# Kernel tuning notes

Measured on AMD Instinct MI355X. Metric: run time of the kernel, lower is better.

The kernel has to match this reference:

```python
import jax, jax.numpy as jnp
import numpy as np

N = 100_000      # nodes
E = 1_600_000    # edges (before self loops)
IN = 128         # in_dim
HID = 64         # hidden_dim (per head)
HEADS = 2
NEG_SLOPE = 0.2  # PyG GATConv default negative_slope


def setup_inputs() -> dict:
    key = jax.random.key(0)
    k = jax.random.split(key, 6)
    x = jax.random.normal(k[0], (N, IN), jnp.float32)
    edge_index = jax.random.randint(k[1], (2, E), 0, N, dtype=jnp.int64)
    # GATConv linear (no bias in lin, bias added after aggregation in PyG)
    W = jax.random.normal(k[2], (IN, HEADS * HID), jnp.float32) * (1.0 / np.sqrt(IN))
    att_src = jax.random.normal(k[3], (HEADS, HID), jnp.float32) * 0.1
    att_dst = jax.random.normal(k[4], (HEADS, HID), jnp.float32) * 0.1
    bias = jnp.zeros((HEADS * HID,), jnp.float32)
    prelu_w = jnp.full((HEADS * HID,), 0.25, jnp.float32)  # nn.PReLU default init
    return {"x": x, "edge_index": edge_index, "W": W, "att_src": att_src,
            "att_dst": att_dst, "bias": bias, "prelu_w": prelu_w}


def reference(x, edge_index, W, att_src, att_dst, bias, prelu_w):
    n = x.shape[0]
    h = (x @ W).reshape(n, HEADS, HID)                 # [N,H,C]
    a_s = jnp.einsum('nhc,hc->nh', h, att_src)         # [N,H]
    a_d = jnp.einsum('nhc,hc->nh', h, att_dst)         # [N,H]
    # add self loops (PyG default add_self_loops=True)
    loops = jnp.arange(n, dtype=edge_index.dtype)
    src = jnp.concatenate([edge_index[0], loops])      # [Et]
    dst = jnp.concatenate([edge_index[1], loops])      # [Et]
    logits = a_s[src] + a_d[dst]                       # [Et,H]
    logits = jnp.where(logits >= 0, logits, NEG_SLOPE * logits)  # LeakyReLU
    # segment softmax over destination neighborhoods
    m = jax.ops.segment_max(logits, dst, num_segments=n)         # [N,H]
    e = jnp.exp(logits - m[dst])
    s = jax.ops.segment_sum(e, dst, num_segments=n)              # [N,H]
    alpha = e / (s[dst] + 1e-16)                                 # [Et,H]
    # (attention dropout p=0.2 is identity in eval mode)
    msg = h[src] * alpha[..., None]                    # [Et,H,C]
    out = jax.ops.segment_sum(msg, dst, num_segments=n).reshape(n, HEADS * HID)
    out = out + bias
    # PReLU with per-channel weight
    return jnp.where(out >= 0, out, prelu_w * out)
```

## Files before the change

kernel.cpp:

```cpp
#include <hip/hip_runtime.h>
#include <hip/hip_fp16.h>
#include <hip/hip_bf16.h>
#include <cstdint>
#include <cstddef>

#define NEG_SLOPE 0.2f
#define BSH 8
#define BNODES 256
#define CAP 5120

typedef __attribute__((ext_vector_type(8))) short short8v;
typedef __attribute__((ext_vector_type(4))) float f32x4;
typedef __attribute__((ext_vector_type(2))) uint32_t u32x2;

__device__ __forceinline__ uint32_t bf16pair(float a, float b) {
    __hip_bfloat162 h = __float22bfloat162_rn(make_float2(a, b));
    return *reinterpret_cast<uint32_t*>(&h);
}
__device__ __forceinline__ uint16_t rne16(float f) {
    uint32_t u = __float_as_uint(f);
    return (uint16_t)((u + 0x7fffu + ((u >> 16) & 1u)) >> 16);
}
__device__ __forceinline__ float bflo(uint32_t u) { return __uint_as_float(u << 16); }
__device__ __forceinline__ float bfhi(uint32_t u) { return __uint_as_float(u & 0xffff0000u); }
__device__ __forceinline__ uint32_t packf16(float a, float b) {
    __half2 h = __floats2half2_rn(a, b);
    return *reinterpret_cast<uint32_t*>(&h);
}

__global__ __launch_bounds__(256, 3) void gemm_scatter(
    const float* __restrict__ x, const float* __restrict__ W,
    const float* __restrict__ att_src, const float* __restrict__ att_dst,
    uint32_t* __restrict__ hb, float* __restrict__ a_s, float* __restrict__ a_d,
    const int* __restrict__ src, const int* __restrict__ dst,
    int* __restrict__ gcur, uint32_t* __restrict__ pairs,
    int e, int nb, int n, int nbs)
{
    constexpr int PW = 136;
    __shared__ __align__(16) char smem[52224];
    const int tid = threadIdx.x;

    if (blockIdx.x < nbs) {
        int* histL  = (int*)smem;
        int* gbaseL = histL + 512;
        const int t0 = blockIdx.x * 4096;

        for (int i = tid; i < nb; i += 256) histL[i] = 0;
        __syncthreads();

        int      myb[16];
        int      myslot[16];
        uint32_t mypk[16];
#pragma unroll 16
        for (int k = 0; k < 16; ++k) {
            int i = t0 + tid + k * 256;
            if (i < e) {
                int s = __builtin_nontemporal_load(src + i);
                int d = __builtin_nontemporal_load(dst + i);
                int b = d >> BSH;
                myb[k]    = b;
                mypk[k]   = (uint32_t)s | ((uint32_t)(d & (BNODES - 1)) << 17);
                myslot[k] = atomicAdd(&histL[b], 1);
            } else myb[k] = -1;
        }
        __syncthreads();
        for (int i = tid; i < nb; i += 256) {
            int c = histL[i];
            gbaseL[i] = c ? atomicAdd(&gcur[i], c) : 0;
        }
        __syncthreads();
#pragma unroll 16
        for (int k = 0; k < 16; ++k) {
            if (myb[k] >= 0) {
                int p = gbaseL[myb[k]] + myslot[k];
                if (p < CAP) pairs[(size_t)myb[k] * CAP + p] = mypk[k];
            }
        }
        return;
    }

    unsigned short* Wt = (unsigned short*)smem;
    unsigned short* Hs = (unsigned short*)(smem + 34816);
    const int w    = tid >> 6;
    const int lane = tid & 63;
    const int cl   = lane & 15;
    const int gq   = lane >> 4;
    const int base = (blockIdx.x - nbs) * 64;

    const float4* W4 = (const float4*)W;
#pragma unroll
    for (int i = 0; i < 8; ++i) {
        int idx = tid + i * 256;
        int k   = (idx >> 5) * 2, c4 = (idx & 31) * 4;
        float4 v0 = W4[k * 32 + (idx & 31)];
        float4 v1 = W4[(k + 1) * 32 + (idx & 31)];
        *(uint32_t*)&Wt[(c4 + 0) * PW + k] = bf16pair(v0.x, v1.x);
        *(uint32_t*)&Wt[(c4 + 1) * PW + k] = bf16pair(v0.y, v1.y);
        *(uint32_t*)&Wt[(c4 + 2) * PW + k] = bf16pair(v0.z, v1.z);
        *(uint32_t*)&Wt[(c4 + 3) * PW + k] = bf16pair(v0.w, v1.w);
    }

    float asr[8], adr[8];
#pragma unroll
    for (int t = 0; t < 8; ++t) {
        asr[t] = att_src[t * 16 + cl];
        adr[t] = att_dst[t * 16 + cl];
    }
    __syncthreads();

    const int rowg = base + w * 16 + cl;
    const int rowc = rowg < n ? rowg : (n - 1);
    const f32x4* xp = (const f32x4*)(x + (size_t)rowc * 128);

    f32x4 acc[8];
#pragma unroll
    for (int t = 0; t < 8; ++t) acc[t] = (f32x4){0.f, 0.f, 0.f, 0.f};

#pragma unroll
    for (int s = 0; s < 4; ++s) {
        int kq = s * 8 + gq * 2;
        f32x4 f0 = __builtin_nontemporal_load(xp + kq);
        f32x4 f1 = __builtin_nontemporal_load(xp + kq + 1);
        union { short8v v; uint32_t d[4]; } A;
        A.d[0] = bf16pair(f0.x, f0.y);
        A.d[1] = bf16pair(f0.z, f0.w);
        A.d[2] = bf16pair(f1.x, f1.y);
        A.d[3] = bf16pair(f1.z, f1.w);
#pragma unroll
        for (int t = 0; t < 8; ++t) {
            union { short8v v; uint4 q; } B;
            B.q = *(const uint4*)&Wt[(t * 16 + cl) * PW + s * 32 + gq * 8];
            acc[t] = __builtin_amdgcn_mfma_f32_16x16x32_bf16(A.v, B.v, acc[t], 0, 0, 0);
        }
    }

    float ps0[4], ps1[4], pd0[4], pd1[4];
#pragma unroll
    for (int r = 0; r < 4; ++r) { ps0[r] = ps1[r] = pd0[r] = pd1[r] = 0.f; }
#pragma unroll
    for (int t = 0; t < 8; ++t) {
#pragma unroll
        for (int r = 0; r < 4; ++r) {
            float v = acc[t][r];
            if (t < 4) { ps0[r] = fmaf(v, asr[t], ps0[r]); pd0[r] = fmaf(v, adr[t], pd0[r]); }
            else       { ps1[r] = fmaf(v, asr[t], ps1[r]); pd1[r] = fmaf(v, adr[t], pd1[r]); }
        }
    }
#pragma unroll
    for (int off = 1; off < 16; off <<= 1) {
#pragma unroll
        for (int r = 0; r < 4; ++r) {
            ps0[r] += __shfl_xor(ps0[r], off);
            ps1[r] += __shfl_xor(ps1[r], off);
            pd0[r] += __shfl_xor(pd0[r], off);
            pd1[r] += __shfl_xor(pd1[r], off);
        }
    }
    if (cl == 0) {
#pragma unroll
        for (int r = 0; r < 4; ++r) {
            int rg = base + w * 16 + gq * 4 + r;
            if (rg < n) {
                a_s[rg * 2 + 0] = ps0[r]; a_s[rg * 2 + 1] = ps1[r];
                a_d[rg * 2 + 0] = pd0[r]; a_d[rg * 2 + 1] = pd1[r];
            }
        }
    }

#pragma unroll
    for (int t = 0; t < 8; ++t) {
#pragma unroll
        for (int r = 0; r < 4; ++r) {
            int row = gq * 4 + r;
            Hs[(size_t)w * 16 * PW + row * PW + t * 16 + cl] = rne16(acc[t][r]);
        }
    }
    __syncthreads();
#pragma unroll
    for (int q = 0; q < 4; ++q) {
        int row = q * 4 + gq;
        int cu  = 4 * cl;
        uint4 v = *(const uint4*)&Hs[(size_t)w * 16 * PW + row * PW + cu * 2];
        int rg = base + w * 16 + row;
        if (rg < n) *(uint4*)&hb[(size_t)rg * 64 + cu] = v;
    }
}

__global__ __launch_bounds__(512) void build_csr(
    const uint32_t* __restrict__ pairs, const int* __restrict__ gcur,
    const float* __restrict__ a_s, const float* __restrict__ a_d,
    uint32_t* __restrict__ meta, uint2* __restrict__ edges, int n, int nb)
{
    __shared__ uint32_t pl[CAP];
    __shared__ int degL[BNODES], curL[BNODES];
    __shared__ float adL[BNODES * 2];
    __shared__ int bscan[512];
    __shared__ int wsum8[8];
    const int b = blockIdx.x, tid = threadIdx.x;
    const int lane = tid & 63, wid = tid >> 6;
    const int nbase = b * BNODES;
    const int nodes = min(BNODES, n - nbase);

    int tot = 0;
    if (tid < nb) {
        int nn = min(BNODES, n - tid * BNODES);
        tot = min(gcur[tid], CAP) + nn;
    }
    int sc = tot;
#pragma unroll
    for (int off = 1; off < 64; off <<= 1) {
        int t = __shfl_up(sc, off);
        if (lane >= off) sc += t;
    }
    if (lane == 63) wsum8[wid] = sc;
    __syncthreads();
    {
        int woff = 0;
#pragma unroll
        for (int k = 0; k < 8; ++k) woff += (k < wid) ? wsum8[k] : 0;
        bscan[tid] = sc + woff;
    }
    if (tid < BNODES) degL[tid] = 1;
    float es0 = 0.f, es1 = 0.f;
    if (tid < nodes) {
        int g = nbase + tid;
        float2 ad = ((const float2*)a_d)[g];
        adL[2 * tid]     = ad.x;
        adL[2 * tid + 1] = ad.y;
        float2 as = ((const float2*)a_s)[g];
        float l0 = as.x + ad.x; l0 = l0 >= 0.f ? l0 : NEG_SLOPE * l0;
        float l1 = as.y + ad.y; l1 = l1 >= 0.f ? l1 : NEG_SLOPE * l1;
        es0 = __expf(l0); es1 = __expf(l1);
    }
    __syncthreads();
    const int C    = min(gcur[b], CAP);
    const int base = bscan[b] - (C + nodes);

    for (int i = tid; i < C; i += 512) {
        uint32_t p = __builtin_nontemporal_load(pairs + (size_t)b * CAP + i);
        pl[i] = p;
        atomicAdd(&degL[p >> 17], 1);
    }
    __syncthreads();

    int v = (tid < nodes) ? degL[tid] : 0;
    int sc2 = v;
#pragma unroll
    for (int off = 1; off < 64; off <<= 1) {
        int t = __shfl_up(sc2, off);
        if (lane >= off) sc2 += t;
    }
    if (lane == 63 && tid < BNODES) wsum8[wid] = sc2;
    __syncthreads();
    int woff2 = 0;
#pragma unroll
    for (int k = 0; k < 4; ++k) woff2 += (k < wid) ? wsum8[k] : 0;
    const int exc = sc2 - v + woff2;

    if (tid < nodes) {
        edges[base + exc] = make_uint2((uint32_t)(nbase + tid), packf16(es0, es1));
        curL[tid] = exc + 1;
        meta[nbase + tid] = (uint32_t)(base + exc) | ((uint32_t)v << 24);
    }
    __syncthreads();
    for (int i = tid; i < C; i += 512) {
        uint32_t p  = pl[i];
        int dl  = p >> 17;
        int s   = p & 0x1FFFF;
        float2 as = ((const float2*)a_s)[s];
        float l0 = as.x + adL[2 * dl];     l0 = l0 >= 0.f ? l0 : NEG_SLOPE * l0;
        float l1 = as.y + adL[2 * dl + 1]; l1 = l1 >= 0.f ? l1 : NEG_SLOPE * l1;
        float e0 = __expf(l0), e1 = __expf(l1);
        int pos = atomicAdd(&curL[dl], 1);
        edges[base + pos] = make_uint2((uint32_t)s, packf16(e0, e1));
    }
}

__global__ __launch_bounds__(256) void attn_agg(
    const uint32_t* __restrict__ hb, const uint2* __restrict__ edges,
    const uint32_t* __restrict__ meta,
    const float* __restrict__ bias, const float* __restrict__ prelu_w,
    float* __restrict__ out, int n)
{
    const int gw   = (blockIdx.x * blockDim.x + threadIdx.x) >> 6;
    const int lane = threadIdx.x & 63;
    if (gw >= n) return;
    const uint32_t mt = meta[gw];
    const int start = (int)(mt & 0xFFFFFFu);
    const int deg   = (int)(mt >> 24);

    if (deg <= 64) {
        int sv = 0; float e0 = 0.f, e1 = 0.f;
        if (lane < deg) {
            u32x2 ed = __builtin_nontemporal_load((const u32x2*)(edges + start + lane));
            sv = (int)ed.x;
            uint32_t ey = ed.y;
            __half2 h2 = *reinterpret_cast<__half2*>(&ey);
            e0 = __half2float(__low2half(h2));
            e1 = __half2float(__high2half(h2));
        }
        float s0 = e0, s1 = e1;
#pragma unroll
        for (int off = 32; off > 0; off >>= 1) {
            s0 += __shfl_xor(s0, off);
            s1 += __shfl_xor(s1, off);
        }
        const float inv0 = 1.f / (s0 + 1e-16f);
        const float inv1 = 1.f / (s1 + 1e-16f);

        const int g = lane >> 4, r = lane & 15;
        float acc[8];
#pragma unroll
        for (int q = 0; q < 8; ++q) acc[q] = 0.f;

        const uint4* hb4 = (const uint4*)hb;
        const int iters = (deg + 15) >> 4;
        for (int jj = 0; jj < iters; ++jj) {
            const int j0 = jj * 16 + g;
            int   s0v = __shfl(sv, j0);
            int   s1v = __shfl(sv, j0 + 4);
            int   s2v = __shfl(sv, j0 + 8);
            int   s3v = __shfl(sv, j0 + 12);
            float A00 = __shfl(e0, j0),      A10 = __shfl(e1, j0);
            float A01 = __shfl(e0, j0 + 4),  A11 = __shfl(e1, j0 + 4);
            float A02 = __shfl(e0, j0 + 8),  A12 = __shfl(e1, j0 + 8);
            float A03 = __shfl(e0, j0 + 12), A13 = __shfl(e1, j0 + 12);
            float Aa = (r < 8) ? A00 : A10;
            float Ab = (r < 8) ? A01 : A11;
            float Ac = (r < 8) ? A02 : A12;
            float Ad = (r < 8) ? A03 : A13;
            uint4 qa = hb4[(size_t)s0v * 16 + r];
            uint4 qb = hb4[(size_t)s1v * 16 + r];
            uint4 qc = hb4[(size_t)s2v * 16 + r];
            uint4 qd = hb4[(size_t)s3v * 16 + r];
            acc[0] = fmaf(Aa, bflo(qa.x), acc[0]); acc[1] = fmaf(Aa, bfhi(qa.x), acc[1]);
            acc[2] = fmaf(Aa, bflo(qa.y), acc[2]); acc[3] = fmaf(Aa, bfhi(qa.y), acc[3]);
            acc[4] = fmaf(Aa, bflo(qa.z), acc[4]); acc[5] = fmaf(Aa, bfhi(qa.z), acc[5]);
            acc[6] = fmaf(Aa, bflo(qa.w), acc[6]); acc[7] = fmaf(Aa, bfhi(qa.w), acc[7]);
            acc[0] = fmaf(Ab, bflo(qb.x), acc[0]); acc[1] = fmaf(Ab, bfhi(qb.x), acc[1]);
            acc[2] = fmaf(Ab, bflo(qb.y), acc[2]); acc[3] = fmaf(Ab, bfhi(qb.y), acc[3]);
            acc[4] = fmaf(Ab, bflo(qb.z), acc[4]); acc[5] = fmaf(Ab, bfhi(qb.z), acc[5]);
            acc[6] = fmaf(Ab, bflo(qb.w), acc[6]); acc[7] = fmaf(Ab, bfhi(qb.w), acc[7]);
            acc[0] = fmaf(Ac, bflo(qc.x), acc[0]); acc[1] = fmaf(Ac, bfhi(qc.x), acc[1]);
            acc[2] = fmaf(Ac, bflo(qc.y), acc[2]); acc[3] = fmaf(Ac, bfhi(qc.y), acc[3]);
            acc[4] = fmaf(Ac, bflo(qc.z), acc[4]); acc[5] = fmaf(Ac, bfhi(qc.z), acc[5]);
            acc[6] = fmaf(Ac, bflo(qc.w), acc[6]); acc[7] = fmaf(Ac, bfhi(qc.w), acc[7]);
            acc[0] = fmaf(Ad, bflo(qd.x), acc[0]); acc[1] = fmaf(Ad, bfhi(qd.x), acc[1]);
            acc[2] = fmaf(Ad, bflo(qd.y), acc[2]); acc[3] = fmaf(Ad, bfhi(qd.y), acc[3]);
            acc[4] = fmaf(Ad, bflo(qd.z), acc[4]); acc[5] = fmaf(Ad, bfhi(qd.z), acc[5]);
            acc[6] = fmaf(Ad, bflo(qd.w), acc[6]); acc[7] = fmaf(Ad, bfhi(qd.w), acc[7]);
        }
#pragma unroll
        for (int q = 0; q < 8; ++q) {
            acc[q] += __shfl_xor(acc[q], 16);
            acc[q] += __shfl_xor(acc[q], 32);
        }
        if (lane < 16) {
            const float winv = (lane < 8) ? inv0 : inv1;
            float4 b0 = ((const float4*)bias)[lane * 2];
            float4 b1 = ((const float4*)bias)[lane * 2 + 1];
            float4 p0 = ((const float4*)prelu_w)[lane * 2];
            float4 p1 = ((const float4*)prelu_w)[lane * 2 + 1];
            f32x4 w0, w1;
            w0.x = fmaf(acc[0], winv, b0.x); w0.x = w0.x >= 0.f ? w0.x : p0.x * w0.x;
            w0.y = fmaf(acc[1], winv, b0.y); w0.y = w0.y >= 0.f ? w0.y : p0.y * w0.y;
            w0.z = fmaf(acc[2], winv, b0.z); w0.z = w0.z >= 0.f ? w0.z : p0.z * w0.z;
            w0.w = fmaf(acc[3], winv, b0.w); w0.w = w0.w >= 0.f ? w0.w : p0.w * w0.w;
            w1.x = fmaf(acc[4], winv, b1.x); w1.x = w1.x >= 0.f ? w1.x : p1.x * w1.x;
            w1.y = fmaf(acc[5], winv, b1.y); w1.y = w1.y >= 0.f ? w1.y : p1.y * w1.y;
            w1.z = fmaf(acc[6], winv, b1.z); w1.z = w1.z >= 0.f ? w1.z : p1.z * w1.z;
            w1.w = fmaf(acc[7], winv, b1.w); w1.w = w1.w >= 0.f ? w1.w : p1.w * w1.w;
            float* op = out + (size_t)gw * 128 + lane * 8;
            __builtin_nontemporal_store(w0, (f32x4*)op);
            __builtin_nontemporal_store(w1, (f32x4*)(op + 4));
        }
    } else {
        float s0 = 0.f, s1 = 0.f;
        for (int t = lane; t < deg; t += 64) {
            uint32_t ey = edges[start + t].y;
            __half2 h2 = *reinterpret_cast<__half2*>(&ey);
            s0 += __half2float(__low2half(h2));
            s1 += __half2float(__high2half(h2));
        }
#pragma unroll
        for (int off = 32; off > 0; off >>= 1) {
            s0 += __shfl_xor(s0, off);
            s1 += __shfl_xor(s1, off);
        }
        const float inv0 = 1.f / (s0 + 1e-16f);
        const float inv1 = 1.f / (s1 + 1e-16f);

        float accL = 0.f, accH = 0.f;
        for (int t0 = 0; t0 < deg; t0 += 64) {
            int tt = t0 + lane;
            int sv = 0; float e0 = 0.f, e1 = 0.f;
            if (tt < deg) {
                uint2 ed = edges[start + tt];
                sv = (int)ed.x;
                __half2 h2 = *reinterpret_cast<__half2*>(&ed.y);
                e0 = __half2float(__low2half(h2));
                e1 = __half2float(__high2half(h2));
            }
            int kmax = min(64, deg - t0);
            for (int j = 0; j < kmax; ++j) {
                int   s  = __shfl(sv, j);
                float A0 = __shfl(e0, j);
                float A1 = __shfl(e1, j);
                float A  = (lane < 32) ? A0 : A1;
                uint32_t u = hb[(size_t)s * 64 + lane];
                accL = fmaf(A, bflo(u), accL);
                accH = fmaf(A, bfhi(u), accH);
            }
        }
        const float winv = (lane < 32) ? inv0 : inv1;
        float2 bz = ((const float2*)bias)[lane];
        float2 pw = ((const float2*)prelu_w)[lane];
        float o0 = fmaf(accL, winv, bz.x), o1 = fmaf(accH, winv, bz.y);
        o0 = o0 >= 0.f ? o0 : pw.x * o0;
        o1 = o1 >= 0.f ? o1 : pw.y * o1;
        float2 rr; rr.x = o0; rr.y = o1;
        ((float2*)out)[(size_t)gw * 64 + lane] = rr;
    }
}

extern "C" void kernel_launch(void* const* d_in, const int* in_sizes, int n_in,
                              void* d_out, int out_size, void* d_ws, size_t ws_size,
                              hipStream_t stream)
{
    const float* x        = (const float*)d_in[0];
    const int*   ei       = (const int*)d_in[1];
    const float* W        = (const float*)d_in[2];
    const float* att_src  = (const float*)d_in[3];
    const float* att_dst  = (const float*)d_in[4];
    const float* bias     = (const float*)d_in[5];
    const float* prelu_w  = (const float*)d_in[6];
    float* out = (float*)d_out;

    const int n = in_sizes[0] / 128;
    const int e = in_sizes[1] / 2;
    const int* srcp = ei;
    const int* dstp = ei + e;
    const int nb  = (n + BNODES - 1) / BNODES;
    const int nbs = (e + 4095) / 4096;
    const int nbg = (n + 63) / 64;

    uint32_t* hb    = (uint32_t*)d_ws;
    uint32_t* meta  = (uint32_t*)(hb + (size_t)n * 64);
    float*    a_s   = (float*)(meta + n);
    float*    a_d   = a_s + (size_t)n * 2;
    int*      gcur  = (int*)(a_d + (size_t)n * 2);
    uint32_t* pairs = (uint32_t*)(gcur + 512);
    uint2*    edges = (uint2*)(pairs + (size_t)nb * CAP);

    hipMemsetAsync(gcur, 0, 512 * sizeof(int), stream);
    gemm_scatter<<<nbs + nbg, 256, 0, stream>>>(x, W, att_src, att_dst,
                                                hb, a_s, a_d, srcp, dstp,
                                                gcur, pairs, e, nb, n, nbs);
    build_csr<<<nb, 512, 0, stream>>>(pairs, gcur, a_s, a_d, meta, edges, n, nb);
    attn_agg<<<(n + 3) / 4, 256, 0, stream>>>(hb, edges, meta, bias, prelu_w, out, n);
}
```

Baseline: 141.4 us.

## Process two destination nodes per wavefront in attention aggregation

```diff
diff --git a/kernel.cpp b/kernel.cpp
--- a/kernel.cpp
+++ b/kernel.cpp
@@ -282,17 +282,22 @@
     const float* __restrict__ bias, const float* __restrict__ prelu_w,
     float* __restrict__ out, int n)
 {
-    const int gw   = (blockIdx.x * blockDim.x + threadIdx.x) >> 6;
+    const int wv   = (blockIdx.x * blockDim.x + threadIdx.x) >> 6;
     const int lane = threadIdx.x & 63;
-    if (gw >= n) return;
-    const uint32_t mt = meta[gw];
+    const int gwA  = wv * 2;
+    if (gwA >= n) return;
+    const int h = lane >> 5, hlane = lane & 31;
+    const int gw = gwA + h;
+    const bool act = gw < n;
+    const uint32_t mt = act ? meta[gw] : 0u;
     const int start = (int)(mt & 0xFFFFFFu);
-    const int deg   = (int)(mt >> 24);
-
-    if (deg <= 64) {
+    const int deg   = act ? (int)(mt >> 24) : 0;
+    const uint4* hb4 = (const uint4*)hb;
+
+    if (__all(deg <= 32)) {
         int sv = 0; float e0 = 0.f, e1 = 0.f;
-        if (lane < deg) {
-            u32x2 ed = __builtin_nontemporal_load((const u32x2*)(edges + start + lane));
+        if (hlane < deg) {
+            u32x2 ed = __builtin_nontemporal_load((const u32x2*)(edges + start + hlane));
             sv = (int)ed.x;
             uint32_t ey = ed.y;
             __half2 h2 = *reinterpret_cast<__half2*>(&ey);
@@ -301,30 +306,30 @@
         }
         float s0 = e0, s1 = e1;
 #pragma unroll
-        for (int off = 32; off > 0; off >>= 1) {
+        for (int off = 16; off > 0; off >>= 1) {
             s0 += __shfl_xor(s0, off);
             s1 += __shfl_xor(s1, off);
         }
         const float inv0 = 1.f / (s0 + 1e-16f);
         const float inv1 = 1.f / (s1 + 1e-16f);
 
-        const int g = lane >> 4, r = lane & 15;
+        const int g = (lane >> 4) & 1, r = lane & 15;
+        const int sbase = h * 32;
         float acc[8];
 #pragma unroll
         for (int q = 0; q < 8; ++q) acc[q] = 0.f;
 
-        const uint4* hb4 = (const uint4*)hb;
-        const int iters = (deg + 15) >> 4;
+        const int iters = (deg + 7) >> 3;
         for (int jj = 0; jj < iters; ++jj) {
-            const int j0 = jj * 16 + g;
-            int   s0v = __shfl(sv, j0);
-            int   s1v = __shfl(sv, j0 + 4);
-            int   s2v = __shfl(sv, j0 + 8);
-            int   s3v = __shfl(sv, j0 + 12);
-            float A00 = __shfl(e0, j0),      A10 = __shfl(e1, j0);
-            float A01 = __shfl(e0, j0 + 4),  A11 = __shfl(e1, j0 + 4);
-            float A02 = __shfl(e0, j0 + 8),  A12 = __shfl(e1, j0 + 8);
-            float A03 = __shfl(e0, j0 + 12), A13 = __shfl(e1, j0 + 12);
+            const int j0 = jj * 8 + g * 4;
+            int   s0v = __shfl(sv, sbase + j0);
+            int   s1v = __shfl(sv, sbase + j0 + 1);
+            int   s2v = __shfl(sv, sbase + j0 + 2);
+            int   s3v = __shfl(sv, sbase + j0 + 3);
+            float A00 = __shfl(e0, sbase + j0),     A10 = __shfl(e1, sbase + j0);
+            float A01 = __shfl(e0, sbase + j0 + 1), A11 = __shfl(e1, sbase + j0 + 1);
+            float A02 = __shfl(e0, sbase + j0 + 2), A12 = __shfl(e1, sbase + j0 + 2);
+            float A03 = __shfl(e0, sbase + j0 + 3), A13 = __shfl(e1, sbase + j0 + 3);
             float Aa = (r < 8) ? A00 : A10;
             float Ab = (r < 8) ? A01 : A11;
             float Ac = (r < 8) ? A02 : A12;
@@ -351,16 +356,14 @@
             acc[6] = fmaf(Ad, bflo(qd.w), acc[6]); acc[7] = fmaf(Ad, bfhi(qd.w), acc[7]);
         }
 #pragma unroll
-        for (int q = 0; q < 8; ++q) {
-            acc[q] += __shfl_xor(acc[q], 16);
-            acc[q] += __shfl_xor(acc[q], 32);
-        }
-        if (lane < 16) {
-            const float winv = (lane < 8) ? inv0 : inv1;
-            float4 b0 = ((const float4*)bias)[lane * 2];
-            float4 b1 = ((const float4*)bias)[lane * 2 + 1];
-            float4 p0 = ((const float4*)prelu_w)[lane * 2];
-            float4 p1 = ((const float4*)prelu_w)[lane * 2 + 1];
+        for (int q = 0; q < 8; ++q) acc[q] += __shfl_xor(acc[q], 16);
+
+        if (hlane < 16 && act) {
+            const float winv = (r < 8) ? inv0 : inv1;
+            float4 b0 = ((const float4*)bias)[r * 2];
+            float4 b1 = ((const float4*)bias)[r * 2 + 1];
+            float4 p0 = ((const float4*)prelu_w)[r * 2];
+            float4 p1 = ((const float4*)prelu_w)[r * 2 + 1];
             f32x4 w0, w1;
             w0.x = fmaf(acc[0], winv, b0.x); w0.x = w0.x >= 0.f ? w0.x : p0.x * w0.x;
             w0.y = fmaf(acc[1], winv, b0.y); w0.y = w0.y >= 0.f ? w0.y : p0.y * w0.y;
@@ -370,56 +373,147 @@
             w1.y = fmaf(acc[5], winv, b1.y); w1.y = w1.y >= 0.f ? w1.y : p1.y * w1.y;
             w1.z = fmaf(acc[6], winv, b1.z); w1.z = w1.z >= 0.f ? w1.z : p1.z * w1.z;
             w1.w = fmaf(acc[7], winv, b1.w); w1.w = w1.w >= 0.f ? w1.w : p1.w * w1.w;
-            float* op = out + (size_t)gw * 128 + lane * 8;
+            float* op = out + (size_t)gw * 128 + r * 8;
             __builtin_nontemporal_store(w0, (f32x4*)op);
             __builtin_nontemporal_store(w1, (f32x4*)(op + 4));
         }
-    } else {
-        float s0 = 0.f, s1 = 0.f;
-        for (int t = lane; t < deg; t += 64) {
-            uint32_t ey = edges[start + t].y;
-            __half2 h2 = *reinterpret_cast<__half2*>(&ey);
-            s0 += __half2float(__low2half(h2));
-            s1 += __half2float(__high2half(h2));
-        }
-#pragma unroll
-        for (int off = 32; off > 0; off >>= 1) {
-            s0 += __shfl_xor(s0, off);
-            s1 += __shfl_xor(s1, off);
-        }
-        const float inv0 = 1.f / (s0 + 1e-16f);
-        const float inv1 = 1.f / (s1 + 1e-16f);
-
-        float accL = 0.f, accH = 0.f;
-        for (int t0 = 0; t0 < deg; t0 += 64) {
-            int tt = t0 + lane;
+        return;
+    }
+
+    for (int pick = 0; pick < 2; ++pick) {
+        const int gwp = gwA + pick;
+        if (gwp >= n) continue;
+        const uint32_t mtp = meta[gwp];
+        const int st  = (int)(mtp & 0xFFFFFFu);
+        const int dg  = (int)(mtp >> 24);
+
+        if (dg <= 64) {
             int sv = 0; float e0 = 0.f, e1 = 0.f;
-            if (tt < deg) {
-                uint2 ed = edges[start + tt];
+            if (lane < dg) {
+                uint2 ed = edges[st + lane];
                 sv = (int)ed.x;
                 __half2 h2 = *reinterpret_cast<__half2*>(&ed.y);
                 e0 = __half2float(__low2half(h2));
                 e1 = __half2float(__high2half(h2));
             }
-            int kmax = min(64, deg - t0);
-            for (int j = 0; j < kmax; ++j) {
-                int   s  = __shfl(sv, j);
-                float A0 = __shfl(e0, j);
-                float A1 = __shfl(e1, j);
-                float A  = (lane < 32) ? A0 : A1;
-                uint32_t u = hb[(size_t)s * 64 + lane];
-                accL = fmaf(A, bflo(u), accL);
-                accH = fmaf(A, bfhi(u), accH);
-            }
-        }
-        const float winv = (lane < 32) ? inv0 : inv1;
-        float2 bz = ((const float2*)bias)[lane];
-        float2 pw = ((const float2*)prelu_w)[lane];
-        float o0 = fmaf(accL, winv, bz.x), o1 = fmaf(accH, winv, bz.y);
-        o0 = o0 >= 0.f ? o0 : pw.x * o0;
-        o1 = o1 >= 0.f ? o1 : pw.y * o1;
-        float2 rr; rr.x = o0; rr.y = o1;
-        ((float2*)out)[(size_t)gw * 64 + lane] = rr;
+            float s0 = e0, s1 = e1;
+#pragma unroll
+            for (int off = 32; off > 0; off >>= 1) {
+                s0 += __shfl_xor(s0, off);
+                s1 += __shfl_xor(s1, off);
+            }
+            const float inv0 = 1.f / (s0 + 1e-16f);
+            const float inv1 = 1.f / (s1 + 1e-16f);
+            const int g = lane >> 4, r = lane & 15;
+            float acc[8];
+#pragma unroll
+            for (int q = 0; q < 8; ++q) acc[q] = 0.f;
+            const int iters = (dg + 15) >> 4;
+            for (int jj = 0; jj < iters; ++jj) {
+                const int j0 = jj * 16 + g;
+                int   s0v = __shfl(sv, j0);
+                int   s1v = __shfl(sv, j0 + 4);
+                int   s2v = __shfl(sv, j0 + 8);
+                int   s3v = __shfl(sv, j0 + 12);
+                float A00 = __shfl(e0, j0),      A10 = __shfl(e1, j0);
+                float A01 = __shfl(e0, j0 + 4),  A11 = __shfl(e1, j0 + 4);
+                float A02 = __shfl(e0, j0 + 8),  A12 = __shfl(e1, j0 + 8);
+                float A03 = __shfl(e0, j0 + 12), A13 = __shfl(e1, j0 + 12);
+                float Aa = (r < 8) ? A00 : A10;
+                float Ab = (r < 8) ? A01 : A11;
+                float Ac = (r < 8) ? A02 : A12;
+                float Ad = (r < 8) ? A03 : A13;
+                uint4 qa = hb4[(size_t)s0v * 16 + r];
+                uint4 qb = hb4[(size_t)s1v * 16 + r];
+                uint4 qc = hb4[(size_t)s2v * 16 + r];
+                uint4 qd = hb4[(size_t)s3v * 16 + r];
+                acc[0] = fmaf(Aa, bflo(qa.x), acc[0]); acc[1] = fmaf(Aa, bfhi(qa.x), acc[1]);
+                acc[2] = fmaf(Aa, bflo(qa.y), acc[2]); acc[3] = fmaf(Aa, bfhi(qa.y), acc[3]);
+                acc[4] = fmaf(Aa, bflo(qa.z), acc[4]); acc[5] = fmaf(Aa, bfhi(qa.z), acc[5]);
+                acc[6] = fmaf(Aa, bflo(qa.w), acc[6]); acc[7] = fmaf(Aa, bfhi(qa.w), acc[7]);
+                acc[0] = fmaf(Ab, bflo(qb.x), acc[0]); acc[1] = fmaf(Ab, bfhi(qb.x), acc[1]);
+                acc[2] = fmaf(Ab, bflo(qb.y), acc[2]); acc[3] = fmaf(Ab, bfhi(qb.y), acc[3]);
+                acc[4] = fmaf(Ab, bflo(qb.z), acc[4]); acc[5] = fmaf(Ab, bfhi(qb.z), acc[5]);
+                acc[6] = fmaf(Ab, bflo(qb.w), acc[6]); acc[7] = fmaf(Ab, bfhi(qb.w), acc[7]);
+                acc[0] = fmaf(Ac, bflo(qc.x), acc[0]); acc[1] = fmaf(Ac, bfhi(qc.x), acc[1]);
+                acc[2] = fmaf(Ac, bflo(qc.y), acc[2]); acc[3] = fmaf(Ac, bfhi(qc.y), acc[3]);
+                acc[4] = fmaf(Ac, bflo(qc.z), acc[4]); acc[5] = fmaf(Ac, bfhi(qc.z), acc[5]);
+                acc[6] = fmaf(Ac, bflo(qc.w), acc[6]); acc[7] = fmaf(Ac, bfhi(qc.w), acc[7]);
+                acc[0] = fmaf(Ad, bflo(qd.x), acc[0]); acc[1] = fmaf(Ad, bfhi(qd.x), acc[1]);
+                acc[2] = fmaf(Ad, bflo(qd.y), acc[2]); acc[3] = fmaf(Ad, bfhi(qd.y), acc[3]);
+                acc[4] = fmaf(Ad, bflo(qd.z), acc[4]); acc[5] = fmaf(Ad, bfhi(qd.z), acc[5]);
+                acc[6] = fmaf(Ad, bflo(qd.w), acc[6]); acc[7] = fmaf(Ad, bfhi(qd.w), acc[7]);
+            }
+#pragma unroll
+            for (int q = 0; q < 8; ++q) {
+                acc[q] += __shfl_xor(acc[q], 16);
+                acc[q] += __shfl_xor(acc[q], 32);
+            }
+            if (lane < 16) {
+                const float winv = (lane < 8) ? inv0 : inv1;
+                float4 b0 = ((const float4*)bias)[lane * 2];
+                float4 b1 = ((const float4*)bias)[lane * 2 + 1];
+                float4 p0 = ((const float4*)prelu_w)[lane * 2];
+                float4 p1 = ((const float4*)prelu_w)[lane * 2 + 1];
+                f32x4 w0, w1;
+                w0.x = fmaf(acc[0], winv, b0.x); w0.x = w0.x >= 0.f ? w0.x : p0.x * w0.x;
+                w0.y = fmaf(acc[1], winv, b0.y); w0.y = w0.y >= 0.f ? w0.y : p0.y * w0.y;
+                w0.z = fmaf(acc[2], winv, b0.z); w0.z = w0.z >= 0.f ? w0.z : p0.z * w0.z;
+                w0.w = fmaf(acc[3], winv, b0.w); w0.w = w0.w >= 0.f ? w0.w : p0.w * w0.w;
+                w1.x = fmaf(acc[4], winv, b1.x); w1.x = w1.x >= 0.f ? w1.x : p1.x * w1.x;
+                w1.y = fmaf(acc[5], winv, b1.y); w1.y = w1.y >= 0.f ? w1.y : p1.y * w1.y;
+                w1.z = fmaf(acc[6], winv, b1.z); w1.z = w1.z >= 0.f ? w1.z : p1.z * w1.z;
+                w1.w = fmaf(acc[7], winv, b1.w); w1.w = w1.w >= 0.f ? w1.w : p1.w * w1.w;
+                float* op = out + (size_t)gwp * 128 + lane * 8;
+                __builtin_nontemporal_store(w0, (f32x4*)op);
+                __builtin_nontemporal_store(w1, (f32x4*)(op + 4));
+            }
+        } else {
+            float s0 = 0.f, s1 = 0.f;
+            for (int t = lane; t < dg; t += 64) {
+                uint32_t ey = edges[st + t].y;
+                __half2 h2 = *reinterpret_cast<__half2*>(&ey);
+                s0 += __half2float(__low2half(h2));
+                s1 += __half2float(__high2half(h2));
+            }
+#pragma unroll
+            for (int off = 32; off > 0; off >>= 1) {
+                s0 += __shfl_xor(s0, off);
+                s1 += __shfl_xor(s1, off);
+            }
+            const float inv0 = 1.f / (s0 + 1e-16f);
+            const float inv1 = 1.f / (s1 + 1e-16f);
+            float accL = 0.f, accH = 0.f;
+            for (int t0 = 0; t0 < dg; t0 += 64) {
+                int tt = t0 + lane;
+                int sv = 0; float e0 = 0.f, e1 = 0.f;
+                if (tt < dg) {
+                    uint2 ed = edges[st + tt];
+                    sv = (int)ed.x;
+                    __half2 h2 = *reinterpret_cast<__half2*>(&ed.y);
+                    e0 = __half2float(__low2half(h2));
+                    e1 = __half2float(__high2half(h2));
+                }
+                int kmax = min(64, dg - t0);
+                for (int j = 0; j < kmax; ++j) {
+                    int   s  = __shfl(sv, j);
+                    float A0 = __shfl(e0, j);
+                    float A1 = __shfl(e1, j);
+                    float A  = (lane < 32) ? A0 : A1;
+                    uint32_t u = hb[(size_t)s * 64 + lane];
+                    accL = fmaf(A, bflo(u), accL);
+                    accH = fmaf(A, bfhi(u), accH);
+                }
+            }
+            const float winv = (lane < 32) ? inv0 : inv1;
+            float2 bz = ((const float2*)bias)[lane];
+            float2 pw = ((const float2*)prelu_w)[lane];
+            float o0 = fmaf(accL, winv, bz.x), o1 = fmaf(accH, winv, bz.y);
+            o0 = o0 >= 0.f ? o0 : pw.x * o0;
+            o1 = o1 >= 0.f ? o1 : pw.y * o1;
+            float2 rr; rr.x = o0; rr.y = o1;
+            ((float2*)out)[(size_t)gwp * 64 + lane] = rr;
+        }
     }
 }
 
@@ -457,5 +551,6 @@
                                                 hb, a_s, a_d, srcp, dstp,
                                                 gcur, pairs, e, nb, n, nbs);
     build_csr<<<nb, 512, 0, stream>>>(pairs, gcur, a_s, a_d, meta, edges, n, nb);
-    attn_agg<<<(n + 3) / 4, 256, 0, stream>>>(hb, edges, meta, bias, prelu_w, out, n);
-}
+    const int nwv = (n + 1) / 2;
+    attn_agg<<<(nwv + 3) / 4, 256, 0, stream>>>(hb, edges, meta, bias, prelu_w, out, n);
+}
```

Measured after the change: 140.0 us. No clear change (-1.0%).
